# Kernel tuning notes

Measured on AMD Instinct MI355X. Metric: run time of the kernel, lower is better.

The kernel has to match this reference:

```python
import jax, jax.numpy as jnp
import numpy as np

SOS = 1  # start-of-sequence token id (module references a global SOS)
VOCAB, EMBED, HIDDEN = 32000, 512, 1024

def setup_inputs() -> dict:
    key = jax.random.key(0)
    ks = jax.random.split(key, 8)
    B = 32
    s = lambda k, shape, scale: jax.random.normal(k, shape, dtype=jnp.float32) * scale
    return {
        "init_hidden": s(ks[0], (1, B, HIDDEN), 1.0),
        "encoder_outputs": s(ks[1], (B, 64, HIDDEN), 1.0),
        "tgt_len": 64,
        "embedding": s(ks[2], (VOCAB, EMBED), 1.0),
        "w_ih": s(ks[3], (3 * HIDDEN, EMBED), 0.03),
        "b_ih": s(ks[4], (3 * HIDDEN,), 0.03),
        "w_hh": s(ks[5], (3 * HIDDEN, HIDDEN), 0.03),
        "b_hh": s(ks[6], (3 * HIDDEN,), 0.03),
        "w_out": s(ks[7], (VOCAB, HIDDEN), 0.03),
        "b_out": jnp.zeros((VOCAB,), dtype=jnp.float32),
    }

def reference(init_hidden, encoder_outputs, tgt_len, embedding, w_ih, b_ih, w_hh, b_hh, w_out, b_out):
    B = init_hidden.shape[1]
    h0 = init_hidden[0]                       # [B, H] (num_layers=1)
    tok0 = jnp.full((B,), SOS, dtype=jnp.int32)

    def step(carry, _):
        h, tok = carry
        x = jnp.tanh(embedding[tok])          # [B, E]
        gi = x @ w_ih.T + b_ih                # [B, 3H]
        gh = h @ w_hh.T + b_hh                # [B, 3H]
        i_r, i_z, i_n = jnp.split(gi, 3, axis=-1)
        h_r, h_z, h_n = jnp.split(gh, 3, axis=-1)
        r = jax.nn.sigmoid(i_r + h_r)
        z = jax.nn.sigmoid(i_z + h_z)
        n = jnp.tanh(i_n + r * h_n)
        h_new = (1.0 - z) * n + z * h         # [B, H]
        logp = jax.nn.log_softmax(h_new @ w_out.T + b_out, axis=-1)  # [B, V]
        tok_new = jnp.argmax(logp, axis=-1).astype(jnp.int32)
        return (h_new, tok_new), logp

    (_, _), outputs = jax.lax.scan(step, (h0, tok0), None, length=tgt_len)
    return outputs                            # [T, B, V] log-probs (matches list of squeezed outputs)
```

## Files before the change

kernel.cpp:

```cpp
#include <hip/hip_runtime.h>
#include <math.h>

#define B    32
#define H    1024
#define EMB  512
#define V    32000
#define SOS  1

#define OFF_X   0
#define OFF_HA  16384
#define OFF_HB  49152
#define OFF_P   81920
#define OFF_C   145920
#define OFF_HHI 147968
#define OFF_HLO 164352
#define OFF_WHI 180736
#define OFF_WLO 16564736

#define NEG_INF (-3.0e38f)

typedef float f4v   __attribute__((ext_vector_type(4)));
typedef short short8v __attribute__((ext_vector_type(8)));
typedef float f32x4 __attribute__((ext_vector_type(4)));

#define MF(a,b,c) c = __builtin_amdgcn_mfma_f32_16x16x32_bf16(a, b, c, 0, 0, 0)

__device__ __forceinline__ unsigned short rnb(float x) {
    unsigned u = __float_as_uint(x);
    unsigned r = u + 0x7FFFu + ((u >> 16) & 1u);
    return (unsigned short)(r >> 16);
}
__device__ __forceinline__ float bfh(unsigned short s) {
    return __uint_as_float(((unsigned)s) << 16);
}
__device__ __forceinline__ void sm_merge(float& m, float& l, int& a,
                                         float om, float ol, int oa)
{
    const bool take = (om > m) || (om == m && oa < a);
    const float mn = take ? om : m;
    const int   an = take ? oa : a;
    l = l * expf(m - mn) + ol * expf(om - mn);
    m = mn; a = an;
}

__global__ void k_init(const float* __restrict__ ih, const float* __restrict__ emb,
                       const float* __restrict__ wout, float* __restrict__ ws)
{
    const size_t idx = (size_t)blockIdx.x * blockDim.x + threadIdx.x;
    const size_t stride = (size_t)gridDim.x * blockDim.x;
    for (size_t i = idx; i < EMB * B; i += stride)
        ws[OFF_X + i] = tanhf(emb[(size_t)SOS * EMB + (i >> 5)]);
    for (size_t i = idx; i < H * B; i += stride) {
        int j = (int)(i >> 5), b = (int)(i & 31);
        ws[OFF_HA + j * 32 + b] = ih[(size_t)b * H + j];
    }
    short* Whi = (short*)(ws + OFF_WHI);
    short* Wlo = (short*)(ws + OFF_WLO);
    for (size_t i = idx; i < (size_t)V * H; i += stride) {
        const float x = wout[i];
        const unsigned short hi = rnb(x);
        Whi[i] = (short)hi;
        Wlo[i] = (short)rnb(x - bfh(hi));
    }
}

__global__ __launch_bounds__(1024) void k_gru(
    const float* __restrict__ xG, const float* __restrict__ hold,
    const float* __restrict__ wih, const float* __restrict__ bih,
    const float* __restrict__ whh, const float* __restrict__ bhh,
    float* __restrict__ hnew, short* __restrict__ Hhi, short* __restrict__ Hlo)
{
    const int t   = threadIdx.x;
    const int blk = blockIdx.x;
    __shared__ float sred[4 * 1152];

    const int ks = t >> 7;
    const int pl = t & 127;
    const int p  = blk * 128 + pl;
    const int b  = p & 31;
    const int j  = p >> 5;

    float ar = 0.f, az = 0.f, ain = 0.f, ahn = 0.f;
    const int k0 = ks * 192, k1 = k0 + 192;

    const int xe = (k1 < EMB) ? k1 : EMB;
    for (int k = k0; k < xe; k += 4) {
        const float u0 = xG[(k + 0) * 32 + b];
        const float u1 = xG[(k + 1) * 32 + b];
        const float u2 = xG[(k + 2) * 32 + b];
        const float u3 = xG[(k + 3) * 32 + b];
        const float4 w0 = *(const float4*)&wih[(size_t)(0 * H + j) * EMB + k];
        const float4 w1 = *(const float4*)&wih[(size_t)(1 * H + j) * EMB + k];
        const float4 w2 = *(const float4*)&wih[(size_t)(2 * H + j) * EMB + k];
        ar  = fmaf(w0.x, u0, fmaf(w0.y, u1, fmaf(w0.z, u2, fmaf(w0.w, u3, ar))));
        az  = fmaf(w1.x, u0, fmaf(w1.y, u1, fmaf(w1.z, u2, fmaf(w1.w, u3, az))));
        ain = fmaf(w2.x, u0, fmaf(w2.y, u1, fmaf(w2.z, u2, fmaf(w2.w, u3, ain))));
    }
    const int hs = (k0 > EMB) ? k0 : EMB;
    for (int k = hs; k < k1; k += 4) {
        const int kh = k - EMB;
        const float u0 = hold[(kh + 0) * 32 + b];
        const float u1 = hold[(kh + 1) * 32 + b];
        const float u2 = hold[(kh + 2) * 32 + b];
        const float u3 = hold[(kh + 3) * 32 + b];
        const float4 w0 = *(const float4*)&whh[(size_t)(0 * H + j) * H + kh];
        const float4 w1 = *(const float4*)&whh[(size_t)(1 * H + j) * H + kh];
        const float4 w2 = *(const float4*)&whh[(size_t)(2 * H + j) * H + kh];
        ar  = fmaf(w0.x, u0, fmaf(w0.y, u1, fmaf(w0.z, u2, fmaf(w0.w, u3, ar))));
        az  = fmaf(w1.x, u0, fmaf(w1.y, u1, fmaf(w1.z, u2, fmaf(w1.w, u3, az))));
        ahn = fmaf(w2.x, u0, fmaf(w2.y, u1, fmaf(w2.z, u2, fmaf(w2.w, u3, ahn))));
    }

    sred[0 * 1152 + pl * 9 + ks] = ar;
    sred[1 * 1152 + pl * 9 + ks] = az;
    sred[2 * 1152 + pl * 9 + ks] = ain;
    sred[3 * 1152 + pl * 9 + ks] = ahn;
    __syncthreads();

    if (t < 128) {
        const int pp = blk * 128 + t;
        const int bb = pp & 31, jj = pp >> 5;
        float s0 = 0.f, s1 = 0.f, s2 = 0.f, s3 = 0.f;
#pragma unroll
        for (int q = 0; q < 8; ++q) {
            s0 += sred[0 * 1152 + t * 9 + q];
            s1 += sred[1 * 1152 + t * 9 + q];
            s2 += sred[2 * 1152 + t * 9 + q];
            s3 += sred[3 * 1152 + t * 9 + q];
        }
        float gr  = s0 + bih[jj]         + bhh[jj];
        float gz  = s1 + bih[H + jj]     + bhh[H + jj];
        float gin = s2 + bih[2 * H + jj];
        float ghn = s3 + bhh[2 * H + jj];
        float r = 1.f / (1.f + expf(-gr));
        float z = 1.f / (1.f + expf(-gz));
        float n = tanhf(gin + r * ghn);
        const int hidx = jj * 32 + bb;
        const float hv = (1.f - z) * n + z * hold[hidx];
        hnew[hidx] = hv;
        const unsigned short hi = rnb(hv);
        const unsigned short lo = rnb(hv - bfh(hi));
        const int pidx = (((jj >> 3) * 32) + bb) * 8 + (jj & 7);
        Hhi[pidx] = (short)hi;
        Hlo[pidx] = (short)lo;
    }
}

__global__ __launch_bounds__(256, 2) void k_proj(
    const short* __restrict__ Whi, const short* __restrict__ Wlo,
    const short* __restrict__ Hhi, const short* __restrict__ Hlo,
    const float* __restrict__ bout, float* __restrict__ orow,
    float4* __restrict__ P)
{
    __shared__ float Red[2 * 32 * 33];
    __shared__ float Dt[32 * 68];
    __shared__ float bl[64];
    __shared__ float pm[2][32], pls[2][32];
    __shared__ int   pa[2][32];

    const int t   = threadIdx.x;
    const int blk = blockIdx.x;
    const int r0  = blk * 64;
    const int w   = t >> 6;
    const int mh  = w >> 1;
    const int kq  = w & 1;
    const int l   = t & 63;
    const int lr  = l & 15;
    const int lg  = l >> 4;

    if (t < 64) bl[t] = bout[r0 + t];

    const short* pAh = Whi + (size_t)(r0 + mh * 32 + lr) * H + lg * 8;
    const short* pAl = Wlo + (size_t)(r0 + mh * 32 + lr) * H + lg * 8;
    const short* pBh = Hhi + ((size_t)lg * 32 + lr) * 8;
    const short* pBl = Hlo + ((size_t)lg * 32 + lr) * 8;

    f32x4 acc00 = {0.f, 0.f, 0.f, 0.f};
    f32x4 acc01 = {0.f, 0.f, 0.f, 0.f};
    f32x4 acc10 = {0.f, 0.f, 0.f, 0.f};
    f32x4 acc11 = {0.f, 0.f, 0.f, 0.f};

#pragma unroll 4
    for (int i = 0; i < 16; ++i) {
        const int c = 2 * i + kq;
        const short8v a0h = *(const short8v*)(pAh + c * 32);
        const short8v a0l = *(const short8v*)(pAl + c * 32);
        const short8v a1h = *(const short8v*)(pAh + 16 * H + c * 32);
        const short8v a1l = *(const short8v*)(pAl + 16 * H + c * 32);
        const short8v b0h = *(const short8v*)(pBh + c * 1024);
        const short8v b0l = *(const short8v*)(pBl + c * 1024);
        const short8v b1h = *(const short8v*)(pBh + c * 1024 + 128);
        const short8v b1l = *(const short8v*)(pBl + c * 1024 + 128);
        MF(a0h, b0h, acc00); MF(a0h, b0l, acc00); MF(a0l, b0h, acc00);
        MF(a0h, b1h, acc01); MF(a0h, b1l, acc01); MF(a0l, b1h, acc01);
        MF(a1h, b0h, acc10); MF(a1h, b0l, acc10); MF(a1l, b0h, acc10);
        MF(a1h, b1h, acc11); MF(a1h, b1l, acc11); MF(a1l, b1h, acc11);
    }

    if (kq == 1) {
#pragma unroll
        for (int mt = 0; mt < 2; ++mt)
#pragma unroll
            for (int r = 0; r < 4; ++r) {
                const int row = mt * 16 + lg * 4 + r;
                Red[mh * 1056 + row * 33 + lr]      = mt ? acc10[r] : acc00[r];
                Red[mh * 1056 + row * 33 + 16 + lr] = mt ? acc11[r] : acc01[r];
            }
    }
    __syncthreads();

    if (kq == 0) {
#pragma unroll
        for (int mt = 0; mt < 2; ++mt)
#pragma unroll
            for (int r = 0; r < 4; ++r) {
                const int row = mt * 16 + lg * 4 + r;
                const float e0 = Red[mh * 1056 + row * 33 + lr];
                const float e1 = Red[mh * 1056 + row * 33 + 16 + lr];
                if (mt) { acc10[r] += e0; acc11[r] += e1; }
                else    { acc00[r] += e0; acc01[r] += e1; }
            }

        float val[2][2][4];
#pragma unroll
        for (int mt = 0; mt < 2; ++mt)
#pragma unroll
            for (int r = 0; r < 4; ++r) {
                const float bo = bl[mh * 32 + mt * 16 + lg * 4 + r];
                val[mt][0][r] = (mt ? acc10[r] : acc00[r]) + bo;
                val[mt][1][r] = (mt ? acc11[r] : acc01[r]) + bo;
            }
#pragma unroll
        for (int mt = 0; mt < 2; ++mt)
#pragma unroll
            for (int nt = 0; nt < 2; ++nt)
#pragma unroll
                for (int r = 0; r < 4; ++r)
                    Dt[(nt * 16 + lr) * 68 + mh * 32 + mt * 16 + lg * 4 + r] = val[mt][nt][r];

#pragma unroll
        for (int nt = 0; nt < 2; ++nt) {
            float m = val[0][nt][0], ls = 1.f;
            int a = r0 + mh * 32 + lg * 4;
#pragma unroll
            for (int q = 1; q < 8; ++q) {
                const int mt = q >> 2, r = q & 3;
                const float x = val[mt][nt][r];
                const int row = r0 + mh * 32 + mt * 16 + lg * 4 + r;
                if (x > m) { ls = ls * expf(m - x) + 1.f; m = x; a = row; }
                else       { ls += expf(x - m); }
            }
            sm_merge(m, ls, a, __shfl_xor(m, 16), __shfl_xor(ls, 16), __shfl_xor(a, 16));
            sm_merge(m, ls, a, __shfl_xor(m, 32), __shfl_xor(ls, 32), __shfl_xor(a, 32));
            if (lg == 0) { pm[mh][nt * 16 + lr] = m; pls[mh][nt * 16 + lr] = ls; pa[mh][nt * 16 + lr] = a; }
        }
    }
    __syncthreads();

    if (t < 32) {
        float m = pm[0][t], ls = pls[0][t]; int a = pa[0][t];
        sm_merge(m, ls, a, pm[1][t], pls[1][t], pa[1][t]);
        P[blk * 32 + t] = make_float4(m, ls, (float)a, 0.f);
    }

    const int sb = t >> 3, rq = t & 7;
#pragma unroll
    for (int hx = 0; hx < 2; ++hx) {
        const f4v v = *(const f4v*)&Dt[sb * 68 + hx * 32 + rq * 4];
        __builtin_nontemporal_store(v,
            (f4v*)&orow[(size_t)sb * V + r0 + hx * 32 + rq * 4]);
    }
}

__global__ __launch_bounds__(256) void k_fin2(
    const float4* __restrict__ partial, const float* __restrict__ emb,
    float* __restrict__ xG, float* __restrict__ C)
{
    const int b = blockIdx.x;
    const int t = threadIdx.x;
    __shared__ float fm[256], fl[256];
    __shared__ int   fa[256], stok;

    float m = NEG_INF, l = 0.f; int a = 0x7FFFFFFF;
    {
        float4 p = partial[t * 32 + b];
        m = p.x; l = p.y; a = (int)p.z;
    }
    if (t + 256 < 500) {
        float4 p = partial[(t + 256) * 32 + b];
        sm_merge(m, l, a, p.x, p.y, (int)p.z);
    }
    fm[t] = m; fl[t] = l; fa[t] = a;
    __syncthreads();
    for (int s = 128; s > 0; s >>= 1) {
        if (t < s) {
            const float om = fm[t + s], ol = fl[t + s];
            const int   oa = fa[t + s];
            float mm = fm[t]; float ll = fl[t]; int aa = fa[t];
            const bool take = (om > mm) || (om == mm && oa < aa);
            const float mn = take ? om : mm;
            const int   an = take ? oa : aa;
            ll = ll * expf(mm - mn) + ol * expf(om - mn);
            fm[t] = mn; fl[t] = ll; fa[t] = an;
        }
        __syncthreads();
    }
    if (t == 0) {
        C[b] = fm[0] + logf(fl[0]);
        stok = fa[0];
    }
    __syncthreads();
    const int TOK = stok;
    for (int k = t; k < EMB; k += 256)
        xG[k * 32 + b] = tanhf(emb[(size_t)TOK * EMB + k]);
}

__global__ __launch_bounds__(256) void k_sub(float* __restrict__ out,
                                             const float* __restrict__ C)
{
    const int r = blockIdx.x;
    const float c = C[r];
    f4v* row = (f4v*)(out + (size_t)r * V);
    for (int v = threadIdx.x; v < V / 4; v += 256) {
        f4v x = __builtin_nontemporal_load(&row[v]);
        x -= c;
        __builtin_nontemporal_store(x, &row[v]);
    }
}

extern "C" void kernel_launch(void* const* d_in, const int* in_sizes, int n_in,
                              void* d_out, int out_size, void* d_ws, size_t ws_size,
                              hipStream_t stream)
{
    const float* p_ih   = (const float*)d_in[0];
    const float* p_emb  = (const float*)d_in[3];
    const float* p_wih  = (const float*)d_in[4];
    const float* p_bih  = (const float*)d_in[5];
    const float* p_whh  = (const float*)d_in[6];
    const float* p_bhh  = (const float*)d_in[7];
    const float* p_wout = (const float*)d_in[8];
    const float* p_bout = (const float*)d_in[9];
    float* out = (float*)d_out;
    float* ws  = (float*)d_ws;
    const int T = out_size / (B * V);

    float*  xG  = ws + OFF_X;
    float*  hA  = ws + OFF_HA;
    float*  hB  = ws + OFF_HB;
    float4* P   = (float4*)(ws + OFF_P);
    float*  C   = ws + OFF_C;
    short*  Hhi = (short*)(ws + OFF_HHI);
    short*  Hlo = (short*)(ws + OFF_HLO);
    short*  Whi = (short*)(ws + OFF_WHI);
    short*  Wlo = (short*)(ws + OFF_WLO);

    k_init<<<2048, 256, 0, stream>>>(p_ih, p_emb, p_wout, ws);

    for (int st = 0; st < T; ++st) {
        float* hold = (st & 1) ? hB : hA;
        float* hnew = (st & 1) ? hA : hB;
        float* orow = out + (size_t)st * B * V;
        k_gru<<<256, 1024, 0, stream>>>(xG, hold, p_wih, p_bih, p_whh, p_bhh,
                                        hnew, Hhi, Hlo);
        k_proj<<<500, 256, 0, stream>>>(Whi, Wlo, Hhi, Hlo, p_bout, orow, P);
        k_fin2<<<B, 256, 0, stream>>>(P, p_emb, xG, C + st * B);
    }
    k_sub<<<T * B, 256, 0, stream>>>(out, C);
}
```

Measured before the change: 3.776 ms.

## Fuse all decode kernels into one persistent cooperative kernel with grid syncs

New measurement: 9.278 ms. +145.7%, slower.

```diff
diff --git a/kernel.cpp b/kernel.cpp
--- a/kernel.cpp
+++ b/kernel.cpp
@@ -1,21 +1,26 @@
 #include <hip/hip_runtime.h>
+#include <hip/hip_cooperative_groups.h>
 #include <math.h>
+
+namespace cg = cooperative_groups;
 
 #define B    32
 #define H    1024
 #define EMB  512
 #define V    32000
 #define SOS  1
+#define NBLK 256
+#define NTHR 1024
 
 #define OFF_X   0
 #define OFF_HA  16384
 #define OFF_HB  49152
 #define OFF_P   81920
-#define OFF_C   145920
-#define OFF_HHI 147968
-#define OFF_HLO 164352
-#define OFF_WHI 180736
-#define OFF_WLO 16564736
+#define OFF_C   113920
+#define OFF_HHI 115968
+#define OFF_HLO 132352
+#define OFF_WHI 148736
+#define OFF_WLO 16532736
 
 #define NEG_INF (-3.0e38f)
 
@@ -43,288 +48,304 @@
     m = mn; a = an;
 }
 
-__global__ void k_init(const float* __restrict__ ih, const float* __restrict__ emb,
-                       const float* __restrict__ wout, float* __restrict__ ws)
+__global__ __launch_bounds__(NTHR, 4) void k_all(
+    const float* __restrict__ ih, const float* __restrict__ emb,
+    const float* __restrict__ wih, const float* __restrict__ bih,
+    const float* __restrict__ whh, const float* __restrict__ bhh,
+    const float* __restrict__ wout, const float* __restrict__ bout,
+    float* __restrict__ out, float* __restrict__ ws, int T)
 {
-    const size_t idx = (size_t)blockIdx.x * blockDim.x + threadIdx.x;
-    const size_t stride = (size_t)gridDim.x * blockDim.x;
-    for (size_t i = idx; i < EMB * B; i += stride)
-        ws[OFF_X + i] = tanhf(emb[(size_t)SOS * EMB + (i >> 5)]);
-    for (size_t i = idx; i < H * B; i += stride) {
+    cg::grid_group grid = cg::this_grid();
+    __shared__ __align__(16) float smem[13184];
+    __shared__ int stok_s;
+
+    const int t   = threadIdx.x;
+    const int blk = blockIdx.x;
+    const size_t gid = (size_t)blk * NTHR + t;
+
+    float*  xG  = ws + OFF_X;
+    float*  hA  = ws + OFF_HA;
+    float*  hB  = ws + OFF_HB;
+    float4* P   = (float4*)(ws + OFF_P);
+    float*  C   = ws + OFF_C;
+    short*  Hhi = (short*)(ws + OFF_HHI);
+    short*  Hlo = (short*)(ws + OFF_HLO);
+    short*  Whi = (short*)(ws + OFF_WHI);
+    short*  Wlo = (short*)(ws + OFF_WLO);
+
+    for (size_t i = gid; i < EMB * B; i += (size_t)NBLK * NTHR)
+        xG[i] = tanhf(emb[(size_t)SOS * EMB + (i >> 5)]);
+    for (size_t i = gid; i < H * B; i += (size_t)NBLK * NTHR) {
         int j = (int)(i >> 5), b = (int)(i & 31);
-        ws[OFF_HA + j * 32 + b] = ih[(size_t)b * H + j];
+        hA[j * 32 + b] = ih[(size_t)b * H + j];
     }
-    short* Whi = (short*)(ws + OFF_WHI);
-    short* Wlo = (short*)(ws + OFF_WLO);
-    for (size_t i = idx; i < (size_t)V * H; i += stride) {
+    for (size_t i = gid; i < (size_t)V * H; i += (size_t)NBLK * NTHR) {
         const float x = wout[i];
         const unsigned short hi = rnb(x);
         Whi[i] = (short)hi;
         Wlo[i] = (short)rnb(x - bfh(hi));
     }
-}
-
-__global__ __launch_bounds__(1024) void k_gru(
-    const float* __restrict__ xG, const float* __restrict__ hold,
-    const float* __restrict__ wih, const float* __restrict__ bih,
-    const float* __restrict__ whh, const float* __restrict__ bhh,
-    float* __restrict__ hnew, short* __restrict__ Hhi, short* __restrict__ Hlo)
-{
-    const int t   = threadIdx.x;
-    const int blk = blockIdx.x;
-    __shared__ float sred[4 * 1152];
-
-    const int ks = t >> 7;
-    const int pl = t & 127;
-    const int p  = blk * 128 + pl;
-    const int b  = p & 31;
-    const int j  = p >> 5;
-
-    float ar = 0.f, az = 0.f, ain = 0.f, ahn = 0.f;
-    const int k0 = ks * 192, k1 = k0 + 192;
-
-    const int xe = (k1 < EMB) ? k1 : EMB;
-    for (int k = k0; k < xe; k += 4) {
-        const float u0 = xG[(k + 0) * 32 + b];
-        const float u1 = xG[(k + 1) * 32 + b];
-        const float u2 = xG[(k + 2) * 32 + b];
-        const float u3 = xG[(k + 3) * 32 + b];
-        const float4 w0 = *(const float4*)&wih[(size_t)(0 * H + j) * EMB + k];
-        const float4 w1 = *(const float4*)&wih[(size_t)(1 * H + j) * EMB + k];
-        const float4 w2 = *(const float4*)&wih[(size_t)(2 * H + j) * EMB + k];
-        ar  = fmaf(w0.x, u0, fmaf(w0.y, u1, fmaf(w0.z, u2, fmaf(w0.w, u3, ar))));
-        az  = fmaf(w1.x, u0, fmaf(w1.y, u1, fmaf(w1.z, u2, fmaf(w1.w, u3, az))));
-        ain = fmaf(w2.x, u0, fmaf(w2.y, u1, fmaf(w2.z, u2, fmaf(w2.w, u3, ain))));
+    grid.sync();
+
+    for (int st = 0; st < T; ++st) {
+        float* hold = (st & 1) ? hB : hA;
+        float* hnew = (st & 1) ? hA : hB;
+        float* orow = out + (size_t)st * B * V;
+
+        {
+            float* sred = smem;
+            const int ks = t >> 7;
+            const int pl = t & 127;
+            const int p  = blk * 128 + pl;
+            const int b  = p & 31;
+            const int j  = p >> 5;
+
+            float ar = 0.f, az = 0.f, ain = 0.f, ahn = 0.f;
+            const int k0 = ks * 192, k1 = k0 + 192;
+
+            const int xe = (k1 < EMB) ? k1 : EMB;
+            for (int k = k0; k < xe; k += 4) {
+                const float u0 = xG[(k + 0) * 32 + b];
+                const float u1 = xG[(k + 1) * 32 + b];
+                const float u2 = xG[(k + 2) * 32 + b];
+                const float u3 = xG[(k + 3) * 32 + b];
+                const float4 w0 = *(const float4*)&wih[(size_t)(0 * H + j) * EMB + k];
+                const float4 w1 = *(const float4*)&wih[(size_t)(1 * H + j) * EMB + k];
+                const float4 w2 = *(const float4*)&wih[(size_t)(2 * H + j) * EMB + k];
+                ar  = fmaf(w0.x, u0, fmaf(w0.y, u1, fmaf(w0.z, u2, fmaf(w0.w, u3, ar))));
+                az  = fmaf(w1.x, u0, fmaf(w1.y, u1, fmaf(w1.z, u2, fmaf(w1.w, u3, az))));
+                ain = fmaf(w2.x, u0, fmaf(w2.y, u1, fmaf(w2.z, u2, fmaf(w2.w, u3, ain))));
+            }
+            const int hs = (k0 > EMB) ? k0 : EMB;
+            for (int k = hs; k < k1; k += 4) {
+                const int kh = k - EMB;
+                const float u0 = hold[(kh + 0) * 32 + b];
+                const float u1 = hold[(kh + 1) * 32 + b];
+                const float u2 = hold[(kh + 2) * 32 + b];
+                const float u3 = hold[(kh + 3) * 32 + b];
+                const float4 w0 = *(const float4*)&whh[(size_t)(0 * H + j) * H + kh];
+                const float4 w1 = *(const float4*)&whh[(size_t)(1 * H + j) * H + kh];
+                const float4 w2 = *(const float4*)&whh[(size_t)(2 * H + j) * H + kh];
+                ar  = fmaf(w0.x, u0, fmaf(w0.y, u1, fmaf(w0.z, u2, fmaf(w0.w, u3, ar))));
+                az  = fmaf(w1.x, u0, fmaf(w1.y, u1, fmaf(w1.z, u2, fmaf(w1.w, u3, az))));
+                ahn = fmaf(w2.x, u0, fmaf(w2.y, u1, fmaf(w2.z, u2, fmaf(w2.w, u3, ahn))));
+            }
+
+            sred[0 * 1152 + pl * 9 + ks] = ar;
+            sred[1 * 1152 + pl * 9 + ks] = az;
+            sred[2 * 1152 + pl * 9 + ks] = ain;
+            sred[3 * 1152 + pl * 9 + ks] = ahn;
+            __syncthreads();
+
+            if (t < 128) {
+                const int pp = blk * 128 + t;
+                const int bb = pp & 31, jj = pp >> 5;
+                float s0 = 0.f, s1 = 0.f, s2 = 0.f, s3 = 0.f;
+#pragma unroll
+                for (int q = 0; q < 8; ++q) {
+                    s0 += sred[0 * 1152 + t * 9 + q];
+                    s1 += sred[1 * 1152 + t * 9 + q];
+                    s2 += sred[2 * 1152 + t * 9 + q];
+                    s3 += sred[3 * 1152 + t * 9 + q];
+                }
+                float gr  = s0 + bih[jj]         + bhh[jj];
+                float gz  = s1 + bih[H + jj]     + bhh[H + jj];
+                float gin = s2 + bih[2 * H + jj];
+                float ghn = s3 + bhh[2 * H + jj];
+                float r = 1.f / (1.f + expf(-gr));
+                float z = 1.f / (1.f + expf(-gz));
+                float n = tanhf(gin + r * ghn);
+                const int hidx = jj * 32 + bb;
+                const float hv = (1.f - z) * n + z * hold[hidx];
+                hnew[hidx] = hv;
+                const unsigned short hi = rnb(hv);
+                const unsigned short lo = rnb(hv - bfh(hi));
+                const int pidx = (((jj >> 3) * 32) + bb) * 8 + (jj & 7);
+                Hhi[pidx] = (short)hi;
+                Hlo[pidx] = (short)lo;
+            }
+        }
+        grid.sync();
+
+        if (blk < 250) {
+            float* Red = smem;
+            float* Dt  = smem + 8448;
+            float* bl  = smem + 12672;
+            float* pm  = smem + 12800;
+            float* pls = smem + 12928;
+            int*   pa  = (int*)(smem + 13056);
+
+            const int r0 = blk * 128;
+            const int w  = t >> 6;
+            const int mh = w >> 2;
+            const int kq = w & 3;
+            const int l  = t & 63;
+            const int lr = l & 15;
+            const int lg = l >> 4;
+
+            if (t < 128) bl[t] = bout[r0 + t];
+
+            const short* pAh = Whi + (size_t)(r0 + mh * 32 + lr) * H + lg * 8;
+            const short* pAl = Wlo + (size_t)(r0 + mh * 32 + lr) * H + lg * 8;
+            const short* pBh = Hhi + ((size_t)lg * 32 + lr) * 8;
+            const short* pBl = Hlo + ((size_t)lg * 32 + lr) * 8;
+
+            f32x4 acc00 = {0.f, 0.f, 0.f, 0.f};
+            f32x4 acc01 = {0.f, 0.f, 0.f, 0.f};
+            f32x4 acc10 = {0.f, 0.f, 0.f, 0.f};
+            f32x4 acc11 = {0.f, 0.f, 0.f, 0.f};
+
+#pragma unroll 2
+            for (int i = 0; i < 8; ++i) {
+                const int c = 4 * i + kq;
+                const short8v a0h = *(const short8v*)(pAh + c * 32);
+                const short8v a0l = *(const short8v*)(pAl + c * 32);
+                const short8v a1h = *(const short8v*)(pAh + 16 * H + c * 32);
+                const short8v a1l = *(const short8v*)(pAl + 16 * H + c * 32);
+                const short8v b0h = *(const short8v*)(pBh + c * 1024);
+                const short8v b0l = *(const short8v*)(pBl + c * 1024);
+                const short8v b1h = *(const short8v*)(pBh + c * 1024 + 128);
+                const short8v b1l = *(const short8v*)(pBl + c * 1024 + 128);
+                MF(a0h, b0h, acc00); MF(a0h, b0l, acc00); MF(a0l, b0h, acc00);
+                MF(a0h, b1h, acc01); MF(a0h, b1l, acc01); MF(a0l, b1h, acc01);
+                MF(a1h, b0h, acc10); MF(a1h, b0l, acc10); MF(a1l, b0h, acc10);
+                MF(a1h, b1h, acc11); MF(a1h, b1l, acc11); MF(a1l, b1h, acc11);
+            }
+
+            if (kq >= 2) {
+                float* rp = Red + (kq - 2) * 4224;
+#pragma unroll
+                for (int mt = 0; mt < 2; ++mt)
+#pragma unroll
+                    for (int r = 0; r < 4; ++r) {
+                        const int row = mh * 32 + mt * 16 + lg * 4 + r;
+                        rp[row * 33 + lr]      = mt ? acc10[r] : acc00[r];
+                        rp[row * 33 + 16 + lr] = mt ? acc11[r] : acc01[r];
+                    }
+            }
+            __syncthreads();
+            if (kq < 2) {
+                const float* rp = Red + kq * 4224;
+#pragma unroll
+                for (int mt = 0; mt < 2; ++mt)
+#pragma unroll
+                    for (int r = 0; r < 4; ++r) {
+                        const int row = mh * 32 + mt * 16 + lg * 4 + r;
+                        const float e0 = rp[row * 33 + lr];
+                        const float e1 = rp[row * 33 + 16 + lr];
+                        if (mt) { acc10[r] += e0; acc11[r] += e1; }
+                        else    { acc00[r] += e0; acc01[r] += e1; }
+                    }
+            }
+            __syncthreads();
+            if (kq == 1) {
+                float* rp = Red;
+#pragma unroll
+                for (int mt = 0; mt < 2; ++mt)
+#pragma unroll
+                    for (int r = 0; r < 4; ++r) {
+                        const int row = mh * 32 + mt * 16 + lg * 4 + r;
+                        rp[row * 33 + lr]      = mt ? acc10[r] : acc00[r];
+                        rp[row * 33 + 16 + lr] = mt ? acc11[r] : acc01[r];
+                    }
+            }
+            __syncthreads();
+            if (kq == 0) {
+                const float* rp = Red;
+                float val[2][2][4];
+#pragma unroll
+                for (int mt = 0; mt < 2; ++mt)
+#pragma unroll
+                    for (int r = 0; r < 4; ++r) {
+                        const int row = mh * 32 + mt * 16 + lg * 4 + r;
+                        const float bo = bl[row];
+                        val[mt][0][r] = (mt ? acc10[r] : acc00[r]) + rp[row * 33 + lr] + bo;
+                        val[mt][1][r] = (mt ? acc11[r] : acc01[r]) + rp[row * 33 + 16 + lr] + bo;
+                    }
+#pragma unroll
+                for (int mt = 0; mt < 2; ++mt)
+#pragma unroll
+                    for (int nt = 0; nt < 2; ++nt)
+#pragma unroll
+                        for (int r = 0; r < 4; ++r)
+                            Dt[(nt * 16 + lr) * 132 + mh * 32 + mt * 16 + lg * 4 + r] = val[mt][nt][r];
+
+#pragma unroll
+                for (int nt = 0; nt < 2; ++nt) {
+                    float m = val[0][nt][0], ls = 1.f;
+                    int a = r0 + mh * 32 + lg * 4;
+#pragma unroll
+                    for (int q = 1; q < 8; ++q) {
+                        const int mt = q >> 2, r = q & 3;
+                        const float x = val[mt][nt][r];
+                        const int row = r0 + mh * 32 + mt * 16 + lg * 4 + r;
+                        if (x > m) { ls = ls * expf(m - x) + 1.f; m = x; a = row; }
+                        else       { ls += expf(x - m); }
+                    }
+                    sm_merge(m, ls, a, __shfl_xor(m, 16), __shfl_xor(ls, 16), __shfl_xor(a, 16));
+                    sm_merge(m, ls, a, __shfl_xor(m, 32), __shfl_xor(ls, 32), __shfl_xor(a, 32));
+                    if (lg == 0) { pm[mh * 32 + nt * 16 + lr] = m; pls[mh * 32 + nt * 16 + lr] = ls; pa[mh * 32 + nt * 16 + lr] = a; }
+                }
+            }
+            __syncthreads();
+
+            if (t < 32) {
+                float m = pm[t], ls = pls[t]; int a = pa[t];
+#pragma unroll
+                for (int q = 1; q < 4; ++q) sm_merge(m, ls, a, pm[q * 32 + t], pls[q * 32 + t], pa[q * 32 + t]);
+                P[blk * 32 + t] = make_float4(m, ls, (float)a, 0.f);
+            }
+            __syncthreads();
+
+            const int sb = t >> 5, rq = t & 31;
+            const f4v v = *(const f4v*)&Dt[sb * 132 + rq * 4];
+            __builtin_nontemporal_store(v, (f4v*)&orow[(size_t)sb * V + r0 + rq * 4]);
+        }
+        grid.sync();
+
+        if (blk < B) {
+            const int b = blk;
+            float* fm = smem;
+            float* fl = smem + 512;
+            int*   fa = (int*)(smem + 1024);
+
+            if (t < 512) {
+                float m = NEG_INF, lsum = 0.f; int a = 0x7FFFFFFF;
+                if (t < 250) {
+                    const float4 p = P[t * 32 + b];
+                    m = p.x; lsum = p.y; a = (int)p.z;
+                }
+                fm[t] = m; fl[t] = lsum; fa[t] = a;
+            }
+            __syncthreads();
+            for (int s = 256; s > 0; s >>= 1) {
+                if (t < s) {
+                    float mm = fm[t]; float ll = fl[t]; int aa = fa[t];
+                    sm_merge(mm, ll, aa, fm[t + s], fl[t + s], fa[t + s]);
+                    fm[t] = mm; fl[t] = ll; fa[t] = aa;
+                }
+                __syncthreads();
+            }
+            if (t == 0) {
+                C[st * 32 + b] = fm[0] + logf(fl[0]);
+                stok_s = fa[0];
+            }
+            __syncthreads();
+            const int TOK = stok_s;
+            if (t < EMB)
+                xG[t * 32 + b] = tanhf(emb[(size_t)TOK * EMB + t]);
+        }
+        grid.sync();
     }
-    const int hs = (k0 > EMB) ? k0 : EMB;
-    for (int k = hs; k < k1; k += 4) {
-        const int kh = k - EMB;
-        const float u0 = hold[(kh + 0) * 32 + b];
-        const float u1 = hold[(kh + 1) * 32 + b];
-        const float u2 = hold[(kh + 2) * 32 + b];
-        const float u3 = hold[(kh + 3) * 32 + b];
-        const float4 w0 = *(const float4*)&whh[(size_t)(0 * H + j) * H + kh];
-        const float4 w1 = *(const float4*)&whh[(size_t)(1 * H + j) * H + kh];
-        const float4 w2 = *(const float4*)&whh[(size_t)(2 * H + j) * H + kh];
-        ar  = fmaf(w0.x, u0, fmaf(w0.y, u1, fmaf(w0.z, u2, fmaf(w0.w, u3, ar))));
-        az  = fmaf(w1.x, u0, fmaf(w1.y, u1, fmaf(w1.z, u2, fmaf(w1.w, u3, az))));
-        ahn = fmaf(w2.x, u0, fmaf(w2.y, u1, fmaf(w2.z, u2, fmaf(w2.w, u3, ahn))));
-    }
-
-    sred[0 * 1152 + pl * 9 + ks] = ar;
-    sred[1 * 1152 + pl * 9 + ks] = az;
-    sred[2 * 1152 + pl * 9 + ks] = ain;
-    sred[3 * 1152 + pl * 9 + ks] = ahn;
-    __syncthreads();
-
-    if (t < 128) {
-        const int pp = blk * 128 + t;
-        const int bb = pp & 31, jj = pp >> 5;
-        float s0 = 0.f, s1 = 0.f, s2 = 0.f, s3 = 0.f;
-#pragma unroll
-        for (int q = 0; q < 8; ++q) {
-            s0 += sred[0 * 1152 + t * 9 + q];
-            s1 += sred[1 * 1152 + t * 9 + q];
-            s2 += sred[2 * 1152 + t * 9 + q];
-            s3 += sred[3 * 1152 + t * 9 + q];
+
+    for (int r = blk; r < T * B; r += NBLK) {
+        const float c = C[r];
+        f4v* row = (f4v*)(out + (size_t)r * V);
+        for (int v = t; v < V / 4; v += NTHR) {
+            f4v x = __builtin_nontemporal_load(&row[v]);
+            x -= c;
+            __builtin_nontemporal_store(x, &row[v]);
         }
-        float gr  = s0 + bih[jj]         + bhh[jj];
-        float gz  = s1 + bih[H + jj]     + bhh[H + jj];
-        float gin = s2 + bih[2 * H + jj];
-        float ghn = s3 + bhh[2 * H + jj];
-        float r = 1.f / (1.f + expf(-gr));
-        float z = 1.f / (1.f + expf(-gz));
-        float n = tanhf(gin + r * ghn);
-        const int hidx = jj * 32 + bb;
-        const float hv = (1.f - z) * n + z * hold[hidx];
-        hnew[hidx] = hv;
-        const unsigned short hi = rnb(hv);
-        const unsigned short lo = rnb(hv - bfh(hi));
-        const int pidx = (((jj >> 3) * 32) + bb) * 8 + (jj & 7);
-        Hhi[pidx] = (short)hi;
-        Hlo[pidx] = (short)lo;
-    }
-}
-
-__global__ __launch_bounds__(256, 2) void k_proj(
-    const short* __restrict__ Whi, const short* __restrict__ Wlo,
-    const short* __restrict__ Hhi, const short* __restrict__ Hlo,
-    const float* __restrict__ bout, float* __restrict__ orow,
-    float4* __restrict__ P)
-{
-    __shared__ float Red[2 * 32 * 33];
-    __shared__ float Dt[32 * 68];
-    __shared__ float bl[64];
-    __shared__ float pm[2][32], pls[2][32];
-    __shared__ int   pa[2][32];
-
-    const int t   = threadIdx.x;
-    const int blk = blockIdx.x;
-    const int r0  = blk * 64;
-    const int w   = t >> 6;
-    const int mh  = w >> 1;
-    const int kq  = w & 1;
-    const int l   = t & 63;
-    const int lr  = l & 15;
-    const int lg  = l >> 4;
-
-    if (t < 64) bl[t] = bout[r0 + t];
-
-    const short* pAh = Whi + (size_t)(r0 + mh * 32 + lr) * H + lg * 8;
-    const short* pAl = Wlo + (size_t)(r0 + mh * 32 + lr) * H + lg * 8;
-    const short* pBh = Hhi + ((size_t)lg * 32 + lr) * 8;
-    const short* pBl = Hlo + ((size_t)lg * 32 + lr) * 8;
-
-    f32x4 acc00 = {0.f, 0.f, 0.f, 0.f};
-    f32x4 acc01 = {0.f, 0.f, 0.f, 0.f};
-    f32x4 acc10 = {0.f, 0.f, 0.f, 0.f};
-    f32x4 acc11 = {0.f, 0.f, 0.f, 0.f};
-
-#pragma unroll 4
-    for (int i = 0; i < 16; ++i) {
-        const int c = 2 * i + kq;
-        const short8v a0h = *(const short8v*)(pAh + c * 32);
-        const short8v a0l = *(const short8v*)(pAl + c * 32);
-        const short8v a1h = *(const short8v*)(pAh + 16 * H + c * 32);
-        const short8v a1l = *(const short8v*)(pAl + 16 * H + c * 32);
-        const short8v b0h = *(const short8v*)(pBh + c * 1024);
-        const short8v b0l = *(const short8v*)(pBl + c * 1024);
-        const short8v b1h = *(const short8v*)(pBh + c * 1024 + 128);
-        const short8v b1l = *(const short8v*)(pBl + c * 1024 + 128);
-        MF(a0h, b0h, acc00); MF(a0h, b0l, acc00); MF(a0l, b0h, acc00);
-        MF(a0h, b1h, acc01); MF(a0h, b1l, acc01); MF(a0l, b1h, acc01);
-        MF(a1h, b0h, acc10); MF(a1h, b0l, acc10); MF(a1l, b0h, acc10);
-        MF(a1h, b1h, acc11); MF(a1h, b1l, acc11); MF(a1l, b1h, acc11);
-    }
-
-    if (kq == 1) {
-#pragma unroll
-        for (int mt = 0; mt < 2; ++mt)
-#pragma unroll
-            for (int r = 0; r < 4; ++r) {
-                const int row = mt * 16 + lg * 4 + r;
-                Red[mh * 1056 + row * 33 + lr]      = mt ? acc10[r] : acc00[r];
-                Red[mh * 1056 + row * 33 + 16 + lr] = mt ? acc11[r] : acc01[r];
-            }
-    }
-    __syncthreads();
-
-    if (kq == 0) {
-#pragma unroll
-        for (int mt = 0; mt < 2; ++mt)
-#pragma unroll
-            for (int r = 0; r < 4; ++r) {
-                const int row = mt * 16 + lg * 4 + r;
-                const float e0 = Red[mh * 1056 + row * 33 + lr];
-                const float e1 = Red[mh * 1056 + row * 33 + 16 + lr];
-                if (mt) { acc10[r] += e0; acc11[r] += e1; }
-                else    { acc00[r] += e0; acc01[r] += e1; }
-            }
-
-        float val[2][2][4];
-#pragma unroll
-        for (int mt = 0; mt < 2; ++mt)
-#pragma unroll
-            for (int r = 0; r < 4; ++r) {
-                const float bo = bl[mh * 32 + mt * 16 + lg * 4 + r];
-                val[mt][0][r] = (mt ? acc10[r] : acc00[r]) + bo;
-                val[mt][1][r] = (mt ? acc11[r] : acc01[r]) + bo;
-            }
-#pragma unroll
-        for (int mt = 0; mt < 2; ++mt)
-#pragma unroll
-            for (int nt = 0; nt < 2; ++nt)
-#pragma unroll
-                for (int r = 0; r < 4; ++r)
-                    Dt[(nt * 16 + lr) * 68 + mh * 32 + mt * 16 + lg * 4 + r] = val[mt][nt][r];
-
-#pragma unroll
-        for (int nt = 0; nt < 2; ++nt) {
-            float m = val[0][nt][0], ls = 1.f;
-            int a = r0 + mh * 32 + lg * 4;
-#pragma unroll
-            for (int q = 1; q < 8; ++q) {
-                const int mt = q >> 2, r = q & 3;
-                const float x = val[mt][nt][r];
-                const int row = r0 + mh * 32 + mt * 16 + lg * 4 + r;
-                if (x > m) { ls = ls * expf(m - x) + 1.f; m = x; a = row; }
-                else       { ls += expf(x - m); }
-            }
-            sm_merge(m, ls, a, __shfl_xor(m, 16), __shfl_xor(ls, 16), __shfl_xor(a, 16));
-            sm_merge(m, ls, a, __shfl_xor(m, 32), __shfl_xor(ls, 32), __shfl_xor(a, 32));
-            if (lg == 0) { pm[mh][nt * 16 + lr] = m; pls[mh][nt * 16 + lr] = ls; pa[mh][nt * 16 + lr] = a; }
-        }
-    }
-    __syncthreads();
-
-    if (t < 32) {
-        float m = pm[0][t], ls = pls[0][t]; int a = pa[0][t];
-        sm_merge(m, ls, a, pm[1][t], pls[1][t], pa[1][t]);
-        P[blk * 32 + t] = make_float4(m, ls, (float)a, 0.f);
-    }
-
-    const int sb = t >> 3, rq = t & 7;
-#pragma unroll
-    for (int hx = 0; hx < 2; ++hx) {
-        const f4v v = *(const f4v*)&Dt[sb * 68 + hx * 32 + rq * 4];
-        __builtin_nontemporal_store(v,
-            (f4v*)&orow[(size_t)sb * V + r0 + hx * 32 + rq * 4]);
-    }
-}
-
-__global__ __launch_bounds__(256) void k_fin2(
-    const float4* __restrict__ partial, const float* __restrict__ emb,
-    float* __restrict__ xG, float* __restrict__ C)
-{
-    const int b = blockIdx.x;
-    const int t = threadIdx.x;
-    __shared__ float fm[256], fl[256];
-    __shared__ int   fa[256], stok;
-
-    float m = NEG_INF, l = 0.f; int a = 0x7FFFFFFF;
-    {
-        float4 p = partial[t * 32 + b];
-        m = p.x; l = p.y; a = (int)p.z;
-    }
-    if (t + 256 < 500) {
-        float4 p = partial[(t + 256) * 32 + b];
-        sm_merge(m, l, a, p.x, p.y, (int)p.z);
-    }
-    fm[t] = m; fl[t] = l; fa[t] = a;
-    __syncthreads();
-    for (int s = 128; s > 0; s >>= 1) {
-        if (t < s) {
-            const float om = fm[t + s], ol = fl[t + s];
-            const int   oa = fa[t + s];
-            float mm = fm[t]; float ll = fl[t]; int aa = fa[t];
-            const bool take = (om > mm) || (om == mm && oa < aa);
-            const float mn = take ? om : mm;
-            const int   an = take ? oa : aa;
-            ll = ll * expf(mm - mn) + ol * expf(om - mn);
-            fm[t] = mn; fl[t] = ll; fa[t] = an;
-        }
-        __syncthreads();
-    }
-    if (t == 0) {
-        C[b] = fm[0] + logf(fl[0]);
-        stok = fa[0];
-    }
-    __syncthreads();
-    const int TOK = stok;
-    for (int k = t; k < EMB; k += 256)
-        xG[k * 32 + b] = tanhf(emb[(size_t)TOK * EMB + k]);
-}
-
-__global__ __launch_bounds__(256) void k_sub(float* __restrict__ out,
-                                             const float* __restrict__ C)
-{
-    const int r = blockIdx.x;
-    const float c = C[r];
-    f4v* row = (f4v*)(out + (size_t)r * V);
-    for (int v = threadIdx.x; v < V / 4; v += 256) {
-        f4v x = __builtin_nontemporal_load(&row[v]);
-        x -= c;
-        __builtin_nontemporal_store(x, &row[v]);
     }
 }
 
@@ -340,30 +361,11 @@
     const float* p_bhh  = (const float*)d_in[7];
     const float* p_wout = (const float*)d_in[8];
     const float* p_bout = (const float*)d_in[9];
-    float* out = (float*)d_out;
-    float* ws  = (float*)d_ws;
-    const int T = out_size / (B * V);
-
-    float*  xG  = ws + OFF_X;
-    float*  hA  = ws + OFF_HA;
-    float*  hB  = ws + OFF_HB;
-    float4* P   = (float4*)(ws + OFF_P);
-    float*  C   = ws + OFF_C;
-    short*  Hhi = (short*)(ws + OFF_HHI);
-    short*  Hlo = (short*)(ws + OFF_HLO);
-    short*  Whi = (short*)(ws + OFF_WHI);
-    short*  Wlo = (short*)(ws + OFF_WLO);
-
-    k_init<<<2048, 256, 0, stream>>>(p_ih, p_emb, p_wout, ws);
-
-    for (int st = 0; st < T; ++st) {
-        float* hold = (st & 1) ? hB : hA;
-        float* hnew = (st & 1) ? hA : hB;
-        float* orow = out + (size_t)st * B * V;
-        k_gru<<<256, 1024, 0, stream>>>(xG, hold, p_wih, p_bih, p_whh, p_bhh,
-                                        hnew, Hhi, Hlo);
-        k_proj<<<500, 256, 0, stream>>>(Whi, Wlo, Hhi, Hlo, p_bout, orow, P);
-        k_fin2<<<B, 256, 0, stream>>>(P, p_emb, xG, C + st * B);
-    }
-    k_sub<<<T * B, 256, 0, stream>>>(out, C);
-}
+    float* p_out = (float*)d_out;
+    float* p_ws  = (float*)d_ws;
+    int T = out_size / (B * V);
+
+    void* args[] = { &p_ih, &p_emb, &p_wih, &p_bih, &p_whh, &p_bhh,
+                     &p_wout, &p_bout, &p_out, &p_ws, &T };
+    hipLaunchCooperativeKernel((void*)k_all, dim3(NBLK), dim3(NTHR), args, 0, stream);
+}
```
